# Optimization experiments

Measured on AMD Instinct MI355X. Metric: run time of the kernel, lower is better.

Reference implementation:

```python
import jax, jax.numpy as jnp
import numpy as np

N = 100000      # n_nodes
E = 1000000     # n_edges (avg degree 10)
D = 64          # input feature dim
LAT = 7         # latent_dim
R = 2           # perturb_rank
H = 2 * LAT     # GCN hidden / dense1 width = 14
P = (LAT + 1) * R  # dense2 width = 16
SP_INV_1 = float(np.log(np.expm1(1.0)))  # softplus_inverse(1.0)


def setup_inputs() -> dict:
    key = jax.random.key(0)
    ks = jax.random.split(key, 10)
    X = jax.random.normal(ks[0], (N, D), dtype=jnp.float32)
    rows = jax.random.randint(ks[1], (E,), 0, N, dtype=jnp.int32)
    cols = jax.random.randint(ks[2], (E,), 0, N, dtype=jnp.int32)
    vals = jax.random.uniform(ks[3], (E,), dtype=jnp.float32)
    s = 0.1
    W1 = jax.random.normal(ks[4], (D, H), dtype=jnp.float32) * s
    W2 = jax.random.normal(ks[5], (H, H), dtype=jnp.float32) * s
    Wd1 = jax.random.normal(ks[6], (H, H), dtype=jnp.float32) * s
    bd1 = jnp.zeros((H,), jnp.float32)
    Wd2 = jax.random.normal(ks[7], (H, P), dtype=jnp.float32) * s
    bd2 = jnp.zeros((P,), jnp.float32)
    return dict(X=X, rows=rows, cols=cols, vals=vals, W1=W1, W2=W2,
                Wd1=Wd1, bd1=bd1, Wd2=Wd2, bd2=bd2)


def reference(X, rows, cols, vals, W1, W2, Wd1, bd1, Wd2, bd2):
    # Sparse adjacency SpMM: (A @ F)[i] = sum_e vals[e] * F[cols[e]] for rows[e]==i
    def spmm(F):
        gathered = vals[:, None] * F[cols]          # [E, d] irregular gather
        return jax.ops.segment_sum(gathered, rows, num_segments=N)

    # GraphConvolution: relu(A @ X @ W)  (keras-gcn order: aggregate then transform)
    h = jax.nn.relu(spmm(X) @ W1)                   # [N, 14]
    h = jax.nn.relu(spmm(h) @ W2)                   # [N, 14]

    param_dist = jnp.tanh(h @ Wd1 + bd1)            # [N, 14]
    param_perturb = jnp.tanh(h @ Wd2 + bd2)         # [N, 16]

    loc = param_dist[:, :LAT]                                      # [N, 7]
    scale_diag = jax.nn.softplus(param_dist[:, LAT:] + SP_INV_1)   # [N, 7]
    perturb_U = param_perturb[:, :LAT * R]                         # [N, 14] (-> [N,7,2])
    perturb_m = param_perturb[:, LAT * R:]                         # [N, 2]

    # MVN-diag-plus-low-rank parameters, concatenated: [N, 7+7+14+2]
    return jnp.concatenate([loc, scale_diag, perturb_U, perturb_m], axis=-1)
```

## Files before the change

kernel.cpp:

```cpp
#include <hip/hip_runtime.h>
#include <hip/hip_fp16.h>
#include <math.h>

constexpr int D     = 64;
constexpr int H     = 14;
constexpr int HP2   = 8;
constexpr int P     = 16;
constexpr int LATc  = 7;
constexpr int OUTW  = 30;
constexpr float SP_INV_1 = 0.5413248546129181f;

__device__ __forceinline__ void pk_atomic_add_f16(__half2* addr, __half2 val) {
    unsigned int bits = *reinterpret_cast<unsigned int*>(&val);
    asm volatile("global_atomic_pk_add_f16 %0, %1, off"
                 :
                 : "v"(addr), "v"(bits)
                 : "memory");
}

__global__ void dense_xw_kernel(const float* __restrict__ X,
                                const float* __restrict__ W1,
                                __half2* __restrict__ XW, int N) {
    __shared__ float w[D * H];
    for (int i = threadIdx.x; i < D * H; i += blockDim.x) w[i] = W1[i];
    __syncthreads();
    int n = blockIdx.x * blockDim.x + threadIdx.x;
    if (n >= N) return;
    float acc[H];
#pragma unroll
    for (int j = 0; j < H; ++j) acc[j] = 0.f;
    const float4* xr = reinterpret_cast<const float4*>(X + (size_t)n * D);
#pragma unroll
    for (int d4 = 0; d4 < D / 4; ++d4) {
        float4 x = xr[d4];
        float xs[4] = {x.x, x.y, x.z, x.w};
#pragma unroll
        for (int k = 0; k < 4; ++k) {
            int d = d4 * 4 + k;
#pragma unroll
            for (int j = 0; j < H; ++j) acc[j] = fmaf(xs[k], w[d * H + j], acc[j]);
        }
    }
    __half2 ov[HP2];
#pragma unroll
    for (int j = 0; j < 7; ++j) ov[j] = __floats2half2_rn(acc[2 * j], acc[2 * j + 1]);
    ov[7] = __floats2half2_rn(0.f, 0.f);
    float4* dst = reinterpret_cast<float4*>(XW + (size_t)n * HP2);
    dst[0] = *reinterpret_cast<float4*>(&ov[0]);
    dst[1] = *reinterpret_cast<float4*>(&ov[4]);
}

__global__ void spmm_pk_kernel(const __half2* __restrict__ F,
                               const int* __restrict__ rows,
                               const int* __restrict__ cols,
                               const float* __restrict__ vals,
                               __half2* __restrict__ Y, int E) {
    int idx = blockIdx.x * blockDim.x + threadIdx.x;
    int e = idx >> 3;
    int f = idx & 7;
    if (e >= E || f >= 7) return;
    int r = rows[e];
    int c = cols[e];
    float v = vals[e];
    float2 xf = __half22float2(F[c * HP2 + f]);
    __half2 p = __floats2half2_rn(v * xf.x, v * xf.y);
    pk_atomic_add_f16(&Y[r * HP2 + f], p);
}

__global__ void dense_hw_kernel(const __half2* __restrict__ Y1,
                                const float* __restrict__ W2,
                                __half2* __restrict__ HW, int N) {
    __shared__ float w[H * H];
    for (int i = threadIdx.x; i < H * H; i += blockDim.x) w[i] = W2[i];
    __syncthreads();
    int n = blockIdx.x * blockDim.x + threadIdx.x;
    if (n >= N) return;
    const float4* yr4 = reinterpret_cast<const float4*>(Y1 + (size_t)n * HP2);
    float4 ya = yr4[0], yb = yr4[1];
    __half2 yh[HP2];
    *reinterpret_cast<float4*>(&yh[0]) = ya;
    *reinterpret_cast<float4*>(&yh[4]) = yb;
    float h[H];
#pragma unroll
    for (int k = 0; k < 7; ++k) {
        float2 t = __half22float2(yh[k]);
        h[2 * k]     = fmaxf(t.x, 0.f);
        h[2 * k + 1] = fmaxf(t.y, 0.f);
    }
    float o[H];
#pragma unroll
    for (int j = 0; j < H; ++j) {
        float a = 0.f;
#pragma unroll
        for (int i = 0; i < H; ++i) a = fmaf(h[i], w[i * H + j], a);
        o[j] = a;
    }
    __half2 ov[HP2];
#pragma unroll
    for (int j = 0; j < 7; ++j) ov[j] = __floats2half2_rn(o[2 * j], o[2 * j + 1]);
    ov[7] = __floats2half2_rn(0.f, 0.f);
    float4* dst = reinterpret_cast<float4*>(HW + (size_t)n * HP2);
    dst[0] = *reinterpret_cast<float4*>(&ov[0]);
    dst[1] = *reinterpret_cast<float4*>(&ov[4]);
}

__global__ void final_kernel(const __half2* __restrict__ Y2,
                             const float* __restrict__ Wd1,
                             const float* __restrict__ bd1,
                             const float* __restrict__ Wd2,
                             const float* __restrict__ bd2,
                             float* __restrict__ out, int N) {
    __shared__ float wd1[H * H], wd2[H * P], b1[H], b2[P];
    for (int i = threadIdx.x; i < H * H; i += blockDim.x) wd1[i] = Wd1[i];
    for (int i = threadIdx.x; i < H * P; i += blockDim.x) wd2[i] = Wd2[i];
    if (threadIdx.x < H) b1[threadIdx.x] = bd1[threadIdx.x];
    if (threadIdx.x < P) b2[threadIdx.x] = bd2[threadIdx.x];
    __syncthreads();
    int n = blockIdx.x * blockDim.x + threadIdx.x;
    if (n >= N) return;

    const float4* yr4 = reinterpret_cast<const float4*>(Y2 + (size_t)n * HP2);
    float4 ya = yr4[0], yb = yr4[1];
    __half2 yh[HP2];
    *reinterpret_cast<float4*>(&yh[0]) = ya;
    *reinterpret_cast<float4*>(&yh[4]) = yb;
    float h[H];
#pragma unroll
    for (int k = 0; k < 7; ++k) {
        float2 t = __half22float2(yh[k]);
        h[2 * k]     = fmaxf(t.x, 0.f);
        h[2 * k + 1] = fmaxf(t.y, 0.f);
    }

    float pd[H];
#pragma unroll
    for (int j = 0; j < H; ++j) {
        float a = b1[j];
#pragma unroll
        for (int i = 0; i < H; ++i) a = fmaf(h[i], wd1[i * H + j], a);
        pd[j] = tanhf(a);
    }
    float pp[P];
#pragma unroll
    for (int j = 0; j < P; ++j) {
        float a = b2[j];
#pragma unroll
        for (int i = 0; i < H; ++i) a = fmaf(h[i], wd2[i * P + j], a);
        pp[j] = tanhf(a);
    }

    float* o = out + (size_t)n * OUTW;
#pragma unroll
    for (int k = 0; k < LATc; ++k) o[k] = pd[k];
#pragma unroll
    for (int k = 0; k < LATc; ++k) {
        float x = pd[LATc + k] + SP_INV_1;
        o[LATc + k] = log1pf(expf(x));
    }
#pragma unroll
    for (int k = 0; k < H; ++k) o[14 + k] = pp[k];
    o[28] = pp[14];
    o[29] = pp[15];
}

extern "C" void kernel_launch(void* const* d_in, const int* in_sizes, int n_in,
                              void* d_out, int out_size, void* d_ws, size_t ws_size,
                              hipStream_t stream) {
    const float* X    = (const float*)d_in[0];
    const int*   rows = (const int*)d_in[1];
    const int*   cols = (const int*)d_in[2];
    const float* vals = (const float*)d_in[3];
    const float* W1   = (const float*)d_in[4];
    const float* W2   = (const float*)d_in[5];
    const float* Wd1  = (const float*)d_in[6];
    const float* bd1  = (const float*)d_in[7];
    const float* Wd2  = (const float*)d_in[8];
    const float* bd2  = (const float*)d_in[9];
    float* out = (float*)d_out;

    const int N = in_sizes[0] / D;
    const int E = in_sizes[1];

    __half2* XW = (__half2*)d_ws;
    __half2* HW = XW + (size_t)N * HP2;
    __half2* Y1 = HW + (size_t)N * HP2;
    __half2* Y2 = Y1 + (size_t)N * HP2;

    (void)hipMemsetAsync(Y1, 0, (size_t)N * HP2 * 2 * sizeof(__half2), stream);

    int blkN = (N + 255) / 256;
    long long spmmThreads = (long long)E * 8;
    unsigned blkS = (unsigned)((spmmThreads + 255) / 256);

    dense_xw_kernel<<<blkN, 256, 0, stream>>>(X, W1, XW, N);
    spmm_pk_kernel<<<blkS, 256, 0, stream>>>(XW, rows, cols, vals, Y1, E);
    dense_hw_kernel<<<blkN, 256, 0, stream>>>(Y1, W2, HW, N);
    spmm_pk_kernel<<<blkS, 256, 0, stream>>>(HW, rows, cols, vals, Y2, E);
    final_kernel<<<blkN, 256, 0, stream>>>(Y2, Wd1, bd1, Wd2, bd2, out, N);
}
```

Before: 221.5 us.

## Fuse all GCN stages into one cooperative persistent kernel with grid syncs

Replaces the memset plus five separate kernel launches with a single cooperative mega-kernel that runs the dense transforms, both SpMM scatter passes and the final head as grid-stride phases separated by grid.sync. Zeroing of the accumulation buffers moves into the first phase, and the weights are loaded into shared memory once per block. The aim is to remove launch overhead and the inter-kernel gaps. In exchange the kernel pays for grid-wide barriers, agent-scope relaxed stores and loads on the intermediates, and a grid capped by occupancy and at 2048 blocks, which may limit the parallelism available to the atomic-heavy SpMM phases. The old multi-kernel path is kept as a fallback if the cooperative launch fails.

```diff
diff --git a/kernel.cpp b/kernel.cpp
--- a/kernel.cpp
+++ b/kernel.cpp
@@ -1,6 +1,9 @@
 #include <hip/hip_runtime.h>
 #include <hip/hip_fp16.h>
+#include <hip/hip_cooperative_groups.h>
 #include <math.h>
+
+namespace cg = cooperative_groups;
 
 constexpr int D     = 64;
 constexpr int H     = 14;
@@ -10,12 +13,183 @@
 constexpr int OUTW  = 30;
 constexpr float SP_INV_1 = 0.5413248546129181f;
 
+constexpr int BLK = 256;
+
 __device__ __forceinline__ void pk_atomic_add_f16(__half2* addr, __half2 val) {
     unsigned int bits = *reinterpret_cast<unsigned int*>(&val);
     asm volatile("global_atomic_pk_add_f16 %0, %1, off"
-                 :
-                 : "v"(addr), "v"(bits)
-                 : "memory");
+                 :: "v"(addr), "v"(bits) : "memory");
+}
+__device__ __forceinline__ void st_agent(unsigned int* p, unsigned int v) {
+    __hip_atomic_store(p, v, __ATOMIC_RELAXED, __HIP_MEMORY_SCOPE_AGENT);
+}
+__device__ __forceinline__ unsigned int ld_agent(const unsigned int* p) {
+    return __hip_atomic_load(p, __ATOMIC_RELAXED, __HIP_MEMORY_SCOPE_AGENT);
+}
+
+__global__ __launch_bounds__(BLK) void mega_kernel(
+        const float* __restrict__ X,
+        const int* __restrict__ rows,
+        const int* __restrict__ cols,
+        const float* __restrict__ vals,
+        const float* __restrict__ W1,
+        const float* __restrict__ W2,
+        const float* __restrict__ Wd1,
+        const float* __restrict__ bd1,
+        const float* __restrict__ Wd2,
+        const float* __restrict__ bd2,
+        float* __restrict__ out,
+        unsigned int* __restrict__ XWu,
+        unsigned int* __restrict__ HWu,
+        unsigned int* __restrict__ Y1u,
+        unsigned int* __restrict__ Y2u,
+        int N, int E) {
+    cg::grid_group grid = cg::this_grid();
+
+    __shared__ float w1[D * H], w2[H * H], wd1[H * H], wd2[H * P], sb1[H], sb2[P];
+    for (int i = threadIdx.x; i < D * H; i += BLK) w1[i] = W1[i];
+    for (int i = threadIdx.x; i < H * H; i += BLK) { w2[i] = W2[i]; wd1[i] = Wd1[i]; }
+    for (int i = threadIdx.x; i < H * P; i += BLK) wd2[i] = Wd2[i];
+    if (threadIdx.x < H) sb1[threadIdx.x] = bd1[threadIdx.x];
+    if (threadIdx.x < P) sb2[threadIdx.x] = bd2[threadIdx.x];
+    __syncthreads();
+
+    const int tid = blockIdx.x * BLK + threadIdx.x;
+    const int nth = gridDim.x * BLK;
+
+    for (int n = tid; n < N; n += nth) {
+        float acc[H];
+#pragma unroll
+        for (int j = 0; j < H; ++j) acc[j] = 0.f;
+        const float4* xr = reinterpret_cast<const float4*>(X + (size_t)n * D);
+#pragma unroll
+        for (int d4 = 0; d4 < D / 4; ++d4) {
+            float4 x = xr[d4];
+            float xs[4] = {x.x, x.y, x.z, x.w};
+#pragma unroll
+            for (int k = 0; k < 4; ++k) {
+                int d = d4 * 4 + k;
+#pragma unroll
+                for (int j = 0; j < H; ++j) acc[j] = fmaf(xs[k], w1[d * H + j], acc[j]);
+            }
+        }
+        unsigned int* xw = XWu + (size_t)n * HP2;
+#pragma unroll
+        for (int j = 0; j < 7; ++j) {
+            __half2 hv = __floats2half2_rn(acc[2 * j], acc[2 * j + 1]);
+            st_agent(&xw[j], *reinterpret_cast<unsigned int*>(&hv));
+        }
+        st_agent(&xw[7], 0u);
+        unsigned int* y1 = Y1u + (size_t)n * HP2;
+        unsigned int* y2 = Y2u + (size_t)n * HP2;
+#pragma unroll
+        for (int j = 0; j < HP2; ++j) { st_agent(&y1[j], 0u); st_agent(&y2[j], 0u); }
+    }
+    __threadfence();
+    grid.sync();
+
+    {
+        const __half2* F = reinterpret_cast<const __half2*>(XWu);
+        __half2* Y = reinterpret_cast<__half2*>(Y1u);
+        long long tot = (long long)E * 8;
+        for (long long i = tid; i < tot; i += nth) {
+            int e = (int)(i >> 3), f = (int)(i & 7);
+            if (f < 7) {
+                int r = rows[e], c = cols[e];
+                float v = vals[e];
+                float2 xf = __half22float2(F[c * HP2 + f]);
+                __half2 p = __floats2half2_rn(v * xf.x, v * xf.y);
+                pk_atomic_add_f16(&Y[r * HP2 + f], p);
+            }
+        }
+    }
+    __threadfence();
+    grid.sync();
+
+    for (int n = tid; n < N; n += nth) {
+        const unsigned int* y1 = Y1u + (size_t)n * HP2;
+        float h[H];
+#pragma unroll
+        for (int k = 0; k < 7; ++k) {
+            unsigned int u = ld_agent(&y1[k]);
+            float2 t = __half22float2(*reinterpret_cast<__half2*>(&u));
+            h[2 * k] = fmaxf(t.x, 0.f);
+            h[2 * k + 1] = fmaxf(t.y, 0.f);
+        }
+        unsigned int* hw = HWu + (size_t)n * HP2;
+#pragma unroll
+        for (int j = 0; j < 7; ++j) {
+            float a0 = 0.f, a1 = 0.f;
+#pragma unroll
+            for (int i = 0; i < H; ++i) {
+                a0 = fmaf(h[i], w2[i * H + 2 * j], a0);
+                a1 = fmaf(h[i], w2[i * H + 2 * j + 1], a1);
+            }
+            __half2 hv = __floats2half2_rn(a0, a1);
+            st_agent(&hw[j], *reinterpret_cast<unsigned int*>(&hv));
+        }
+        st_agent(&hw[7], 0u);
+    }
+    __threadfence();
+    grid.sync();
+
+    {
+        const __half2* F = reinterpret_cast<const __half2*>(HWu);
+        __half2* Y = reinterpret_cast<__half2*>(Y2u);
+        long long tot = (long long)E * 8;
+        for (long long i = tid; i < tot; i += nth) {
+            int e = (int)(i >> 3), f = (int)(i & 7);
+            if (f < 7) {
+                int r = rows[e], c = cols[e];
+                float v = vals[e];
+                float2 xf = __half22float2(F[c * HP2 + f]);
+                __half2 p = __floats2half2_rn(v * xf.x, v * xf.y);
+                pk_atomic_add_f16(&Y[r * HP2 + f], p);
+            }
+        }
+    }
+    __threadfence();
+    grid.sync();
+
+    for (int n = tid; n < N; n += nth) {
+        const unsigned int* y2 = Y2u + (size_t)n * HP2;
+        float h[H];
+#pragma unroll
+        for (int k = 0; k < 7; ++k) {
+            unsigned int u = ld_agent(&y2[k]);
+            float2 t = __half22float2(*reinterpret_cast<__half2*>(&u));
+            h[2 * k] = fmaxf(t.x, 0.f);
+            h[2 * k + 1] = fmaxf(t.y, 0.f);
+        }
+        float pd[H];
+#pragma unroll
+        for (int j = 0; j < H; ++j) {
+            float a = sb1[j];
+#pragma unroll
+            for (int i = 0; i < H; ++i) a = fmaf(h[i], wd1[i * H + j], a);
+            pd[j] = tanhf(a);
+        }
+        float pp[P];
+#pragma unroll
+        for (int j = 0; j < P; ++j) {
+            float a = sb2[j];
+#pragma unroll
+            for (int i = 0; i < H; ++i) a = fmaf(h[i], wd2[i * P + j], a);
+            pp[j] = tanhf(a);
+        }
+        float* o = out + (size_t)n * OUTW;
+#pragma unroll
+        for (int k = 0; k < LATc; ++k) o[k] = pd[k];
+#pragma unroll
+        for (int k = 0; k < LATc; ++k) {
+            float x = pd[LATc + k] + SP_INV_1;
+            o[LATc + k] = log1pf(expf(x));
+        }
+#pragma unroll
+        for (int k = 0; k < H; ++k) o[14 + k] = pp[k];
+        o[28] = pp[14];
+        o[29] = pp[15];
+    }
 }
 
 __global__ void dense_xw_kernel(const float* __restrict__ X,
@@ -178,13 +352,37 @@
     const float* bd2  = (const float*)d_in[9];
     float* out = (float*)d_out;
 
-    const int N = in_sizes[0] / D;
-    const int E = in_sizes[1];
-
-    __half2* XW = (__half2*)d_ws;
-    __half2* HW = XW + (size_t)N * HP2;
-    __half2* Y1 = HW + (size_t)N * HP2;
-    __half2* Y2 = Y1 + (size_t)N * HP2;
+    int N = in_sizes[0] / D;
+    int E = in_sizes[1];
+
+    unsigned int* XWu = (unsigned int*)d_ws;
+    unsigned int* HWu = XWu + (size_t)N * HP2;
+    unsigned int* Y1u = HWu + (size_t)N * HP2;
+    unsigned int* Y2u = Y1u + (size_t)N * HP2;
+
+    int blocksPerCU = 0;
+    hipError_t qerr = hipOccupancyMaxActiveBlocksPerMultiprocessor(
+        &blocksPerCU, (const void*)mega_kernel, BLK, 0);
+    int numCU = 0;
+    hipError_t aerr = hipDeviceGetAttribute(&numCU,
+        hipDeviceAttributeMultiprocessorCount, 0);
+
+    bool coop_ok = (qerr == hipSuccess && aerr == hipSuccess && blocksPerCU > 0 && numCU > 0);
+    if (coop_ok) {
+        int grid = blocksPerCU * numCU;
+        if (grid > 2048) grid = 2048;
+        void* args[] = {&X, &rows, &cols, &vals, &W1, &W2, &Wd1, &bd1, &Wd2, &bd2,
+                        &out, &XWu, &HWu, &Y1u, &Y2u, &N, &E};
+        hipError_t lerr = hipLaunchCooperativeKernel((const void*)mega_kernel,
+                                                     dim3(grid), dim3(BLK),
+                                                     args, 0, stream);
+        if (lerr == hipSuccess) return;
+    }
+
+    __half2* XW = (__half2*)XWu;
+    __half2* HW = (__half2*)HWu;
+    __half2* Y1 = (__half2*)Y1u;
+    __half2* Y2 = (__half2*)Y2u;
 
     (void)hipMemsetAsync(Y1, 0, (size_t)N * HP2 * 2 * sizeof(__half2), stream);
 
```

New measurement: 225.0 us. No clear change (+1.6%).

## Fuse accumulator zeroing into dense kernel, split rows across thread pairs, stage output in LDS

Applied to the files above, without the earlier changes.

Removes the separate memset by having the first dense kernel zero both SpMM accumulators, saving one launch and one pass over the buffers. It splits each node's 64-wide dot product across two threads combined with a shuffle, which doubles the parallelism of that X-read-bound kernel. The final kernel now stages its 30-float rows in shared memory and writes them out with coalesced stores, replacing strided per-thread stores. The cost is a large LDS allocation (about 30KB per block) that may limit occupancy.

```diff
diff --git a/kernel.cpp b/kernel.cpp
--- a/kernel.cpp
+++ b/kernel.cpp
@@ -13,41 +13,57 @@
 __device__ __forceinline__ void pk_atomic_add_f16(__half2* addr, __half2 val) {
     unsigned int bits = *reinterpret_cast<unsigned int*>(&val);
     asm volatile("global_atomic_pk_add_f16 %0, %1, off"
-                 :
-                 : "v"(addr), "v"(bits)
-                 : "memory");
+                 :: "v"(addr), "v"(bits) : "memory");
 }
 
 __global__ void dense_xw_kernel(const float* __restrict__ X,
                                 const float* __restrict__ W1,
-                                __half2* __restrict__ XW, int N) {
+                                __half2* __restrict__ XW,
+                                __half2* __restrict__ Y1,
+                                __half2* __restrict__ Y2, int N) {
     __shared__ float w[D * H];
     for (int i = threadIdx.x; i < D * H; i += blockDim.x) w[i] = W1[i];
     __syncthreads();
-    int n = blockIdx.x * blockDim.x + threadIdx.x;
+    int t = blockIdx.x * blockDim.x + threadIdx.x;
+    int n = t >> 1;
+    int half = t & 1;
     if (n >= N) return;
+
     float acc[H];
 #pragma unroll
     for (int j = 0; j < H; ++j) acc[j] = 0.f;
-    const float4* xr = reinterpret_cast<const float4*>(X + (size_t)n * D);
-#pragma unroll
-    for (int d4 = 0; d4 < D / 4; ++d4) {
+    const float4* xr = reinterpret_cast<const float4*>(X + (size_t)n * D) + half * 8;
+#pragma unroll
+    for (int d4 = 0; d4 < 8; ++d4) {
         float4 x = xr[d4];
         float xs[4] = {x.x, x.y, x.z, x.w};
 #pragma unroll
         for (int k = 0; k < 4; ++k) {
-            int d = d4 * 4 + k;
+            int d = half * 32 + d4 * 4 + k;
 #pragma unroll
             for (int j = 0; j < H; ++j) acc[j] = fmaf(xs[k], w[d * H + j], acc[j]);
         }
     }
-    __half2 ov[HP2];
-#pragma unroll
-    for (int j = 0; j < 7; ++j) ov[j] = __floats2half2_rn(acc[2 * j], acc[2 * j + 1]);
-    ov[7] = __floats2half2_rn(0.f, 0.f);
-    float4* dst = reinterpret_cast<float4*>(XW + (size_t)n * HP2);
-    dst[0] = *reinterpret_cast<float4*>(&ov[0]);
-    dst[1] = *reinterpret_cast<float4*>(&ov[4]);
+#pragma unroll
+    for (int j = 0; j < H; ++j) acc[j] += __shfl_xor(acc[j], 1);
+
+    __half2 ov[4];
+    if (half == 0) {
+        ov[0] = __floats2half2_rn(acc[0], acc[1]);
+        ov[1] = __floats2half2_rn(acc[2], acc[3]);
+        ov[2] = __floats2half2_rn(acc[4], acc[5]);
+        ov[3] = __floats2half2_rn(acc[6], acc[7]);
+    } else {
+        ov[0] = __floats2half2_rn(acc[8], acc[9]);
+        ov[1] = __floats2half2_rn(acc[10], acc[11]);
+        ov[2] = __floats2half2_rn(acc[12], acc[13]);
+        ov[3] = __floats2half2_rn(0.f, 0.f);
+    }
+    reinterpret_cast<float4*>(XW + (size_t)n * HP2)[half] = *reinterpret_cast<float4*>(ov);
+
+    float4 z = make_float4(0.f, 0.f, 0.f, 0.f);
+    reinterpret_cast<float4*>(Y1 + (size_t)n * HP2)[half] = z;
+    reinterpret_cast<float4*>(Y2 + (size_t)n * HP2)[half] = z;
 }
 
 __global__ void spmm_pk_kernel(const __half2* __restrict__ F,
@@ -104,63 +120,68 @@
     dst[1] = *reinterpret_cast<float4*>(&ov[4]);
 }
 
-__global__ void final_kernel(const __half2* __restrict__ Y2,
-                             const float* __restrict__ Wd1,
-                             const float* __restrict__ bd1,
-                             const float* __restrict__ Wd2,
-                             const float* __restrict__ bd2,
-                             float* __restrict__ out, int N) {
+__global__ __launch_bounds__(256) void final_kernel(
+        const __half2* __restrict__ Y2,
+        const float* __restrict__ Wd1,
+        const float* __restrict__ bd1,
+        const float* __restrict__ Wd2,
+        const float* __restrict__ bd2,
+        float* __restrict__ out, int N) {
     __shared__ float wd1[H * H], wd2[H * P], b1[H], b2[P];
-    for (int i = threadIdx.x; i < H * H; i += blockDim.x) wd1[i] = Wd1[i];
-    for (int i = threadIdx.x; i < H * P; i += blockDim.x) wd2[i] = Wd2[i];
+    __shared__ float so[256 * OUTW];
+    for (int i = threadIdx.x; i < H * H; i += 256) wd1[i] = Wd1[i];
+    for (int i = threadIdx.x; i < H * P; i += 256) wd2[i] = Wd2[i];
     if (threadIdx.x < H) b1[threadIdx.x] = bd1[threadIdx.x];
     if (threadIdx.x < P) b2[threadIdx.x] = bd2[threadIdx.x];
     __syncthreads();
-    int n = blockIdx.x * blockDim.x + threadIdx.x;
-    if (n >= N) return;
-
-    const float4* yr4 = reinterpret_cast<const float4*>(Y2 + (size_t)n * HP2);
-    float4 ya = yr4[0], yb = yr4[1];
-    __half2 yh[HP2];
-    *reinterpret_cast<float4*>(&yh[0]) = ya;
-    *reinterpret_cast<float4*>(&yh[4]) = yb;
-    float h[H];
-#pragma unroll
-    for (int k = 0; k < 7; ++k) {
-        float2 t = __half22float2(yh[k]);
-        h[2 * k]     = fmaxf(t.x, 0.f);
-        h[2 * k + 1] = fmaxf(t.y, 0.f);
-    }
-
-    float pd[H];
-#pragma unroll
-    for (int j = 0; j < H; ++j) {
-        float a = b1[j];
-#pragma unroll
-        for (int i = 0; i < H; ++i) a = fmaf(h[i], wd1[i * H + j], a);
-        pd[j] = tanhf(a);
-    }
-    float pp[P];
-#pragma unroll
-    for (int j = 0; j < P; ++j) {
-        float a = b2[j];
-#pragma unroll
-        for (int i = 0; i < H; ++i) a = fmaf(h[i], wd2[i * P + j], a);
-        pp[j] = tanhf(a);
-    }
-
-    float* o = out + (size_t)n * OUTW;
-#pragma unroll
-    for (int k = 0; k < LATc; ++k) o[k] = pd[k];
-#pragma unroll
-    for (int k = 0; k < LATc; ++k) {
-        float x = pd[LATc + k] + SP_INV_1;
-        o[LATc + k] = log1pf(expf(x));
-    }
-#pragma unroll
-    for (int k = 0; k < H; ++k) o[14 + k] = pp[k];
-    o[28] = pp[14];
-    o[29] = pp[15];
+
+    int base = blockIdx.x * 256;
+    int n = base + threadIdx.x;
+    if (n < N) {
+        const float4* yr4 = reinterpret_cast<const float4*>(Y2 + (size_t)n * HP2);
+        float4 ya = yr4[0], yb = yr4[1];
+        __half2 yh[HP2];
+        *reinterpret_cast<float4*>(&yh[0]) = ya;
+        *reinterpret_cast<float4*>(&yh[4]) = yb;
+        float h[H];
+#pragma unroll
+        for (int k = 0; k < 7; ++k) {
+            float2 t = __half22float2(yh[k]);
+            h[2 * k]     = fmaxf(t.x, 0.f);
+            h[2 * k + 1] = fmaxf(t.y, 0.f);
+        }
+        float* so_row = &so[threadIdx.x * OUTW];
+        float pd7[LATc];
+#pragma unroll
+        for (int j = 0; j < H; ++j) {
+            float a = b1[j];
+#pragma unroll
+            for (int i = 0; i < H; ++i) a = fmaf(h[i], wd1[i * H + j], a);
+            float t = tanhf(a);
+            if (j < LATc) so_row[j] = t;
+            else pd7[j - LATc] = t;
+        }
+#pragma unroll
+        for (int k = 0; k < LATc; ++k) {
+            float x = pd7[k] + SP_INV_1;
+            so_row[LATc + k] = log1pf(expf(x));
+        }
+#pragma unroll
+        for (int j = 0; j < P; ++j) {
+            float a = b2[j];
+#pragma unroll
+            for (int i = 0; i < H; ++i) a = fmaf(h[i], wd2[i * P + j], a);
+            so_row[14 + j] = tanhf(a);
+        }
+    }
+    __syncthreads();
+
+    int rowsHere = N - base;
+    if (rowsHere > 256) rowsHere = 256;
+    if (rowsHere < 0) rowsHere = 0;
+    int cnt = rowsHere * OUTW;
+    float* obase = out + (size_t)base * OUTW;
+    for (int i = threadIdx.x; i < cnt; i += 256) obase[i] = so[i];
 }
 
 extern "C" void kernel_launch(void* const* d_in, const int* in_sizes, int n_in,
@@ -186,13 +207,12 @@
     __half2* Y1 = HW + (size_t)N * HP2;
     __half2* Y2 = Y1 + (size_t)N * HP2;
 
-    (void)hipMemsetAsync(Y1, 0, (size_t)N * HP2 * 2 * sizeof(__half2), stream);
-
-    int blkN = (N + 255) / 256;
+    int blkN  = (N + 255) / 256;
+    int blkN2 = (2 * N + 255) / 256;
     long long spmmThreads = (long long)E * 8;
     unsigned blkS = (unsigned)((spmmThreads + 255) / 256);
 
-    dense_xw_kernel<<<blkN, 256, 0, stream>>>(X, W1, XW, N);
+    dense_xw_kernel<<<blkN2, 256, 0, stream>>>(X, W1, XW, Y1, Y2, N);
     spmm_pk_kernel<<<blkS, 256, 0, stream>>>(XW, rows, cols, vals, Y1, E);
     dense_hw_kernel<<<blkN, 256, 0, stream>>>(Y1, W2, HW, N);
     spmm_pk_kernel<<<blkS, 256, 0, stream>>>(HW, rows, cols, vals, Y2, E);
```

After: 219.0 us. No clear change (-1.1%).
